# Optimization experiments

Measured on AMD Instinct MI355X. Metric: run time of the kernel, lower is better.

Reference implementation:

```python
import jax, jax.numpy as jnp
import numpy as np

D_MODEL = 512
N_HEADS = 8
MAX_CH = 128
LN_EPS = 1e-5


def setup_inputs() -> dict:
    key = jax.random.key(0)
    ks = jax.random.split(key, 8)
    B, T, C, D = 8, 256, 64, D_MODEL
    x = jax.random.normal(ks[0], (B, T, C, D), dtype=jnp.float32)
    # nn.MultiheadAttention params: packed in_proj [3D, D], out_proj [D, D]
    in_proj_w = jax.random.normal(ks[1], (3 * D, D), dtype=jnp.float32) * 0.02
    in_proj_b = jnp.zeros((3 * D,), dtype=jnp.float32)
    out_proj_w = jax.random.normal(ks[2], (D, D), dtype=jnp.float32) * 0.02
    out_proj_b = jnp.zeros((D,), dtype=jnp.float32)
    ln_g = jnp.ones((D,), dtype=jnp.float32)
    ln_b = jnp.zeros((D,), dtype=jnp.float32)
    rel_pos_bias = jax.random.normal(ks[3], (N_HEADS, MAX_CH, MAX_CH), dtype=jnp.float32) * 0.02
    return {"x": x, "in_proj_w": in_proj_w, "in_proj_b": in_proj_b,
            "out_proj_w": out_proj_w, "out_proj_b": out_proj_b,
            "ln_g": ln_g, "ln_b": ln_b, "rel_pos_bias": rel_pos_bias}


def _layernorm(x, g, b):
    mu = jnp.mean(x, axis=-1, keepdims=True)
    var = jnp.var(x, axis=-1, keepdims=True)
    return (x - mu) * jax.lax.rsqrt(var + LN_EPS) * g + b


def reference(x, in_proj_w, in_proj_b, out_proj_w, out_proj_b, ln_g, ln_b, rel_pos_bias):
    B, T, C, D = x.shape
    H = N_HEADS
    hd = D // H
    N = B * T
    xf = x.reshape(N, C, D)
    # 2D additive attn_mask: mean over heads of rel-pos bias, broadcast over heads/batch
    bias = jnp.mean(rel_pos_bias[:, :C, :C], axis=0)  # [C, C]
    qkv = xf @ in_proj_w.T + in_proj_b  # [N, C, 3D]
    q, k, v = jnp.split(qkv, 3, axis=-1)
    q = q.reshape(N, C, H, hd)
    k = k.reshape(N, C, H, hd)
    v = v.reshape(N, C, H, hd)
    scores = jnp.einsum('nqhd,nkhd->nhqk', q, k) / jnp.sqrt(jnp.float32(hd))
    scores = scores + bias[None, None, :, :]
    attn = jax.nn.softmax(scores, axis=-1)
    ctx = jnp.einsum('nhqk,nkhd->nqhd', attn, v).reshape(N, C, D)
    attn_out = ctx @ out_proj_w.T + out_proj_b
    out = _layernorm(xf + attn_out, ln_g, ln_b)
    return out.reshape(B, T, C, D)
```

## Files before the change

kernel.cpp:

```cpp
#include <hip/hip_runtime.h>
#include <stdint.h>
#include <stddef.h>


typedef __attribute__((ext_vector_type(8))) short short8;
typedef __attribute__((ext_vector_type(4))) float f32x4;

typedef __attribute__((address_space(3))) unsigned int as3_u32;
typedef __attribute__((address_space(1))) unsigned int as1_u32;

#define VMCNT12 asm volatile("s_waitcnt vmcnt(12)" ::: "memory")
#define VMCNT8 asm volatile("s_waitcnt vmcnt(8)" ::: "memory")
#define VMCNT5 asm volatile("s_waitcnt vmcnt(5)" ::: "memory")
#define VMCNT4 asm volatile("s_waitcnt vmcnt(4)" ::: "memory")
#define VMCNT0 asm volatile("s_waitcnt vmcnt(0)" ::: "memory")
#define LGKM0  asm volatile("s_waitcnt lgkmcnt(0)" ::: "memory")
#define BARR() __builtin_amdgcn_s_barrier()
#define PRIO1  __builtin_amdgcn_s_setprio(1)
#define PRIO0  __builtin_amdgcn_s_setprio(0)

__device__ __forceinline__ unsigned short f2bf(float f) {
  unsigned u = __builtin_bit_cast(unsigned, f);
  u = (u + 0x7FFFu + ((u >> 16) & 1u)) >> 16;
  return (unsigned short)u;
}

__device__ __forceinline__ f32x4 mfma16(short8 a, short8 b, f32x4 c) {
  return __builtin_amdgcn_mfma_f32_16x16x32_bf16(a, b, c, 0, 0, 0);
}

__device__ __forceinline__ short8 rd8s(const char* buf, int row, int unit) {
  return *(const short8*)(buf + row * 128 + ((unit ^ (row & 7)) * 16));
}
__device__ __forceinline__ void wr2s(char* buf, int row, int col, unsigned short v) {
  int slot = (col >> 3) ^ (row & 7);
  *(unsigned short*)(buf + row * 128 + slot * 16 + (col & 7) * 2) = v;
}
__device__ __forceinline__ void wr8s(char* buf, int row, int col, uint2 v) {
  int slot = (col >> 3) ^ (row & 7);
  *(uint2*)(buf + row * 128 + slot * 16 + (col & 7) * 2) = v;
}

__device__ __forceinline__ void stage16k(char* ldsbase, const char* gsrc, int w, int lane) {
#pragma unroll
  for (int j = 0; j < 4; ++j) {
    int off = j * 4096 + w * 1024;
    __builtin_amdgcn_global_load_lds((const as1_u32*)(gsrc + off + lane * 16),
                                     (as3_u32*)(ldsbase + off), 16, 0, 0);
  }
}

__device__ __forceinline__ void load_xq(short8* xq, const char* xqbase,
                                        int wm, int l15, int g) {
#pragma unroll
  for (int mt = 0; mt < 2; ++mt)
#pragma unroll
    for (int ks = 0; ks < 4; ++ks) {
      int row = wm * 32 + mt * 16 + l15;
      int u = ks * 4 + g;
      xq[mt * 4 + ks] = *(const short8*)(xqbase + u * 1024 + row * 16);
    }
}

__device__ __forceinline__ void proj_body(const char* ws, const short8* xq,
                                          int wn, int l15, int g, f32x4 acc[2][2]) {
  PRIO1;
#pragma unroll
  for (int ks = 0; ks < 4; ++ks)
#pragma unroll
    for (int nt = 0; nt < 2; ++nt) {
      int row = wn * 32 + nt * 16 + l15;
      int kg = ks * 4 + g;
      int us = (kg & 8) | ((kg ^ row) & 7);
      short8 bfr = *(const short8*)(ws + row * 256 + us * 16);
      acc[0][nt] = mfma16(xq[ks], bfr, acc[0][nt]);
      acc[1][nt] = mfma16(xq[4 + ks], bfr, acc[1][nt]);
    }
  PRIO0;
}

__global__ void prep_kernel(const float* __restrict__ x,
                            const float* __restrict__ wqkv_f,
                            const float* __restrict__ wo_f,
                            const float* __restrict__ rel,
                            unsigned short* __restrict__ wt,
                            float* __restrict__ bias2d,
                            char* __restrict__ dout) {
  int b = blockIdx.x, tid = threadIdx.x;
  if (b < 8192) {
    int n = b >> 2, kc = b & 3;
    unsigned short* dst =
        (unsigned short*)(dout + (size_t)n * 131072 + 65536 + kc * 16384);
    const float* src0 = x + (size_t)n * 32768 + kc * 128;
#pragma unroll
    for (int t = 0; t < 4; ++t) {
      int row = t * 16 + (tid >> 4);
      int u = tid & 15;
      const float* src = src0 + row * 512 + u * 8;
      float4 a = *(const float4*)src;
      float4 c = *(const float4*)(src + 4);
      unsigned p0 = (unsigned)f2bf(a.x) | ((unsigned)f2bf(a.y) << 16);
      unsigned p1 = (unsigned)f2bf(a.z) | ((unsigned)f2bf(a.w) << 16);
      unsigned p2 = (unsigned)f2bf(c.x) | ((unsigned)f2bf(c.y) << 16);
      unsigned p3 = (unsigned)f2bf(c.z) | ((unsigned)f2bf(c.w) << 16);
      *(uint4*)(dst + (u * 64 + row) * 8) = make_uint4(p0, p1, p2, p3);
    }
  } else if (b < 8320) {
    int cb = b - 8192;
    unsigned short* dst = wt + (size_t)cb * 8192;
#pragma unroll
    for (int t = 0; t < 4; ++t) {
      int u = t * 256 + tid;
      int row = u >> 4, us = u & 15;
      int kg = (us & 8) | ((us ^ row) & 7);
      const float* src;
      if (cb < 96) {
        int h = cb / 12, j = cb % 12;
        int kc = j / 3, rg = j % 3;
        src = wqkv_f + (size_t)(rg * 512 + h * 64 + row) * 512 + kc * 128 + kg * 8;
      } else {
        int cw = cb - 96;
        int kc = cw >> 3, ng = cw & 7;
        src = wo_f + (size_t)(ng * 64 + row) * 512 + kc * 128 + kg * 8;
      }
      float4 a = *(const float4*)src;
      float4 c = *(const float4*)(src + 4);
      unsigned p0 = (unsigned)f2bf(a.x) | ((unsigned)f2bf(a.y) << 16);
      unsigned p1 = (unsigned)f2bf(a.z) | ((unsigned)f2bf(a.w) << 16);
      unsigned p2 = (unsigned)f2bf(c.x) | ((unsigned)f2bf(c.y) << 16);
      unsigned p3 = (unsigned)f2bf(c.z) | ((unsigned)f2bf(c.w) << 16);
      *(uint4*)(dst + u * 8) = make_uint4(p0, p1, p2, p3);
    }
  } else {
    int idx = (b - 8320) * 256 + tid;
    int m = idx >> 6, nn = idx & 63;
    float s = 0.f;
#pragma unroll
    for (int hh = 0; hh < 8; ++hh) s += rel[hh * 16384 + m * 128 + nn];
    bias2d[idx] = s * 0.125f;
  }
}

__global__ __launch_bounds__(256, 2) void attn_qkv(
    const char* __restrict__ wq,
    const float* __restrict__ bqkv,
    const float* __restrict__ bias2d,
    char* __restrict__ ctxg) {
  extern __shared__ __attribute__((aligned(16))) char smem[];
  char* WR = smem;
  char* B0 = smem + 49152;
  char* B1 = smem + 57344;
  char* B2 = smem + 65536;
  float* BQ = (float*)(smem + 73728);

  const int n = blockIdx.x;
  const int tid = threadIdx.x;
  const int w = tid >> 6, lane = tid & 63;
  const int l15 = lane & 15, g = lane >> 4;
  const int wm = w >> 1, wn = w & 1;
  const int mrow = w * 16 + g * 4;
  const int wrow = w * 16 + l15;

  const char* xsrc = ctxg + (size_t)n * 131072 + 65536;

#pragma unroll
  for (int i = 0; i < 6; ++i) BQ[i * 256 + tid] = bqkv[i * 256 + tid];
  float b2d[16];
#pragma unroll
  for (int nt = 0; nt < 4; ++nt)
#pragma unroll
    for (int r = 0; r < 4; ++r)
      b2d[nt * 4 + r] = bias2d[(mrow + r) * 64 + nt * 16 + l15];
  VMCNT0; LGKM0; BARR();

  short8 xq[8];
  load_xq(xq, xsrc, wm, l15, g);
  stage16k(WR, wq, w, lane);

  for (int h = 0; h < 8; ++h) {
    f32x4 aq[2][2] = {}, ak[2][2] = {}, av[2][2] = {};
#pragma unroll
    for (int kc = 0; kc < 4; ++kc) {
      const int j = h * 12 + kc * 3;
      stage16k(WR + 16384, wq + (size_t)(j + 1) * 16384, w, lane);
      if (h == 0 && kc == 0) { VMCNT4; } else { VMCNT12; }
      BARR();
      proj_body(WR, xq, wn, l15, g, aq);
      stage16k(WR + 32768, wq + (size_t)(j + 2) * 16384, w, lane);
      VMCNT4; BARR();
      proj_body(WR + 16384, xq, wn, l15, g, ak);
      if (j + 3 < 96) {
        stage16k(WR, wq + (size_t)(j + 3) * 16384, w, lane);
        VMCNT4;
      } else {
        VMCNT0;
      }
      BARR();
      proj_body(WR + 32768, xq, wn, l15, g, av);
      if (!(h == 7 && kc == 3))
        load_xq(xq, xsrc + (size_t)((kc + 1) & 3) * 16384, wm, l15, g);
    }

    {
      float bq2[2], bk2[2], bv2[2];
#pragma unroll
      for (int nt = 0; nt < 2; ++nt) {
        int col = h * 64 + wn * 32 + nt * 16 + l15;
        bq2[nt] = BQ[col];
        bk2[nt] = BQ[512 + col];
        bv2[nt] = BQ[1024 + col];
      }
#pragma unroll
      for (int mt = 0; mt < 2; ++mt)
#pragma unroll
        for (int nt = 0; nt < 2; ++nt) {
          int rowb = wm * 32 + mt * 16 + g * 4;
          int col = wn * 32 + nt * 16 + l15;
#pragma unroll
          for (int r = 0; r < 4; ++r) {
            wr2s(B0, rowb + r, col, f2bf(aq[mt][nt][r] + bq2[nt]));
            wr2s(B1, rowb + r, col, f2bf(ak[mt][nt][r] + bk2[nt]));
          }
          unsigned short p0 = f2bf(av[mt][nt][0] + bv2[nt]);
          unsigned short p1 = f2bf(av[mt][nt][1] + bv2[nt]);
          unsigned short p2 = f2bf(av[mt][nt][2] + bv2[nt]);
          unsigned short p3 = f2bf(av[mt][nt][3] + bv2[nt]);
          unsigned lo = (unsigned)p0 | ((unsigned)p1 << 16);
          unsigned hi = (unsigned)p2 | ((unsigned)p3 << 16);
          wr8s(B2, col, rowb, make_uint2(lo, hi));
        }
    }
    LGKM0; BARR();

    {
      f32x4 sc[4] = {};
      short8 aq0 = rd8s(B0, wrow, g);
      short8 aq1 = rd8s(B0, wrow, 4 + g);
#pragma unroll
      for (int nt = 0; nt < 4; ++nt)
        sc[nt] = mfma16(aq0, rd8s(B1, nt * 16 + l15, g), sc[nt]);
#pragma unroll
      for (int nt = 0; nt < 4; ++nt)
        sc[nt] = mfma16(aq1, rd8s(B1, nt * 16 + l15, 4 + g), sc[nt]);
      float mx[4] = {-1e30f, -1e30f, -1e30f, -1e30f};
#pragma unroll
      for (int nt = 0; nt < 4; ++nt)
#pragma unroll
        for (int r = 0; r < 4; ++r) {
          float v = sc[nt][r] * 0.125f + b2d[nt * 4 + r];
          sc[nt][r] = v;
          mx[r] = fmaxf(mx[r], v);
        }
#pragma unroll
      for (int mk = 1; mk < 16; mk <<= 1)
#pragma unroll
        for (int r = 0; r < 4; ++r) mx[r] = fmaxf(mx[r], __shfl_xor(mx[r], mk));
      float sm[4] = {0.f, 0.f, 0.f, 0.f};
#pragma unroll
      for (int nt = 0; nt < 4; ++nt)
#pragma unroll
        for (int r = 0; r < 4; ++r) {
          float e = __expf(sc[nt][r] - mx[r]);
          sc[nt][r] = e;
          sm[r] += e;
        }
#pragma unroll
      for (int mk = 1; mk < 16; mk <<= 1)
#pragma unroll
        for (int r = 0; r < 4; ++r) sm[r] += __shfl_xor(sm[r], mk);
      float inv[4];
#pragma unroll
      for (int r = 0; r < 4; ++r) inv[r] = 1.0f / sm[r];
#pragma unroll
      for (int nt = 0; nt < 4; ++nt)
#pragma unroll
        for (int r = 0; r < 4; ++r)
          wr2s(B0, mrow + r, nt * 16 + l15, f2bf(sc[nt][r] * inv[r]));
    }

    f32x4 cv[4] = {};
    {
      short8 ap0 = rd8s(B0, wrow, g);
      short8 ap1 = rd8s(B0, wrow, 4 + g);
#pragma unroll
      for (int nt = 0; nt < 4; ++nt)
        cv[nt] = mfma16(ap0, rd8s(B2, nt * 16 + l15, g), cv[nt]);
#pragma unroll
      for (int nt = 0; nt < 4; ++nt)
        cv[nt] = mfma16(ap1, rd8s(B2, nt * 16 + l15, 4 + g), cv[nt]);
    }
    BARR();
#pragma unroll
    for (int nt = 0; nt < 4; ++nt)
#pragma unroll
      for (int r = 0; r < 4; ++r)
        wr2s(B1, mrow + r, nt * 16 + l15, f2bf(cv[nt][r]));
    LGKM0; BARR();

    {
      char* cdst = ctxg + (size_t)n * 131072 + h * 8192;
#pragma unroll
      for (int it = 0; it < 2; ++it) {
        int flat = it * 256 + tid;
        int row = flat >> 3, s = flat & 7;
        uint4 v = *(const uint4*)(B1 + row * 128 + s * 16);
        *(uint4*)(cdst + row * 128 + s * 16) = v;
      }
    }
  }
}

__global__ __launch_bounds__(256, 2) void oproj_ln(
    const char* __restrict__ ctxg,
    const char* __restrict__ wo,
    const float* __restrict__ bo,
    const float* __restrict__ x,
    const float* __restrict__ lng,
    const float* __restrict__ lnb,
    float* __restrict__ out) {
  __shared__ __attribute__((aligned(16))) char smem[65536];
  char* WB = smem;
  char* CB = smem + 32768;
  float* EP  = (float*)smem;
  float* SM1 = (float*)(smem + 32768);
  float* SM2 = (float*)(smem + 33408);

  const int n = blockIdx.x;
  const int tid = threadIdx.x;
  const int w = tid >> 6, lane = tid & 63;
  const int l15 = lane & 15, g = lane >> 4;
  const int um = w >> 1, un = w & 1;

  const char* cbase = ctxg + (size_t)n * 131072;

  stage16k(CB, cbase, w, lane);
  stage16k(WB, wo, w, lane);

  f32x4 acc[8][2][2] = {};

  for (int kc = 0; kc < 4; ++kc) {
    short8 actx[2][4];
#pragma unroll
    for (int ng = 0; ng < 8; ++ng) {
      int b = kc * 8 + ng;
      if (b < 31)
        stage16k(WB + (((b + 1) & 1) << 14), wo + (size_t)(b + 1) * 16384, w, lane);
      if ((ng & 1) == 0 && kc < 3) {
        int p = ng >> 1;
        int off = p * 4096 + w * 1024;
        __builtin_amdgcn_global_load_lds(
            (const as1_u32*)(cbase + (kc + 1) * 16384 + off + lane * 16),
            (as3_u32*)(CB + (((kc + 1) & 1) << 14) + off), 16, 0, 0);
      }
      if (b < 31) { VMCNT5; } else { VMCNT0; }
      BARR();
      const char* cb = CB + ((kc & 1) << 14);
      if (ng == 0) {
#pragma unroll
        for (int mt = 0; mt < 2; ++mt)
#pragma unroll
          for (int ks = 0; ks < 4; ++ks) {
            int row = um * 32 + mt * 16 + l15;
            int u = ks * 4 + g;
            actx[mt][ks] = *(const short8*)(cb + (u >> 3) * 8192 + row * 128 +
                                            (((u & 7) ^ (row & 7)) * 16));
          }
      }
      const char* ws = WB + ((b & 1) << 14);
      PRIO1;
#pragma unroll
      for (int ks = 0; ks < 4; ++ks) {
#pragma unroll
        for (int nt = 0; nt < 2; ++nt) {
          int row = un * 32 + nt * 16 + l15;
          int kg = ks * 4 + g;
          int us = (kg & 8) | ((kg ^ row) & 7);
          short8 bfr = *(const short8*)(ws + row * 256 + us * 16);
          acc[ng][0][nt] = mfma16(actx[0][ks], bfr, acc[ng][0][nt]);
          acc[ng][1][nt] = mfma16(actx[1][ks], bfr, acc[ng][1][nt]);
        }
      }
      PRIO0;
      BARR();
    }
  }

  VMCNT0;
  const float* xblk = x + (size_t)n * 32768;
  float* oblk = out + (size_t)n * 32768;
  float s1[2][4] = {}, s2[2][4] = {};

#pragma unroll
  for (int ng = 0; ng < 8; ++ng) {
#pragma unroll
    for (int t = 0; t < 4; ++t) {
      int flat = t * 256 + tid;
      int row = flat >> 4, f4 = flat & 15;
      float4 v = *(const float4*)(xblk + row * 512 + ng * 64 + f4 * 4);
      *(float4*)(EP + row * 68 + f4 * 4) = v;
    }
    LGKM0; BARR();
    float boA[2];
#pragma unroll
    for (int nt = 0; nt < 2; ++nt) boA[nt] = bo[ng * 64 + un * 32 + nt * 16 + l15];
#pragma unroll
    for (int mt = 0; mt < 2; ++mt)
#pragma unroll
      for (int nt = 0; nt < 2; ++nt)
#pragma unroll
        for (int r = 0; r < 4; ++r) {
          int row = um * 32 + mt * 16 + g * 4 + r;
          float xv = EP[row * 68 + un * 32 + nt * 16 + l15];
          float v = acc[ng][mt][nt][r] + boA[nt] + xv;
          acc[ng][mt][nt][r] = v;
          s1[mt][r] += v;
          s2[mt][r] += v * v;
        }
    LGKM0; BARR();
  }
#pragma unroll
  for (int mk = 1; mk < 16; mk <<= 1)
#pragma unroll
    for (int mt = 0; mt < 2; ++mt)
#pragma unroll
      for (int r = 0; r < 4; ++r) {
        s1[mt][r] += __shfl_xor(s1[mt][r], mk);
        s2[mt][r] += __shfl_xor(s2[mt][r], mk);
      }
  if (l15 == 0) {
#pragma unroll
    for (int mt = 0; mt < 2; ++mt)
#pragma unroll
      for (int r = 0; r < 4; ++r) {
        int row = um * 32 + mt * 16 + g * 4 + r;
        SM1[row * 2 + un] = s1[mt][r];
        SM2[row * 2 + un] = s2[mt][r];
      }
  }
  LGKM0; BARR();
  float mu[2][4], rs[2][4];
#pragma unroll
  for (int mt = 0; mt < 2; ++mt)
#pragma unroll
    for (int r = 0; r < 4; ++r) {
      int row = um * 32 + mt * 16 + g * 4 + r;
      float a1 = SM1[row * 2] + SM1[row * 2 + 1];
      float a2 = SM2[row * 2] + SM2[row * 2 + 1];
      float m = a1 * (1.0f / 512.0f);
      float var = a2 * (1.0f / 512.0f) - m * m;
      mu[mt][r] = m;
      rs[mt][r] = rsqrtf(var + 1e-5f);
    }
  BARR();
#pragma unroll
  for (int ng = 0; ng < 8; ++ng) {
    float lgA[2], lbA[2];
#pragma unroll
    for (int nt = 0; nt < 2; ++nt) {
      int col = ng * 64 + un * 32 + nt * 16 + l15;
      lgA[nt] = lng[col];
      lbA[nt] = lnb[col];
    }
#pragma unroll
    for (int mt = 0; mt < 2; ++mt)
#pragma unroll
      for (int nt = 0; nt < 2; ++nt)
#pragma unroll
        for (int r = 0; r < 4; ++r) {
          int row = um * 32 + mt * 16 + g * 4 + r;
          EP[row * 68 + un * 32 + nt * 16 + l15] =
              (acc[ng][mt][nt][r] - mu[mt][r]) * rs[mt][r] * lgA[nt] + lbA[nt];
        }
    LGKM0; BARR();
#pragma unroll
    for (int t = 0; t < 4; ++t) {
      int flat = t * 256 + tid;
      int row = flat >> 4, f4 = flat & 15;
      *(float4*)(oblk + row * 512 + ng * 64 + f4 * 4) =
          *(const float4*)(EP + row * 68 + f4 * 4);
    }
    BARR();
  }
}

extern "C" void kernel_launch(void* const* d_in, const int* in_sizes, int n_in,
                              void* d_out, int out_size, void* d_ws, size_t ws_size,
                              hipStream_t stream) {
  const float* x    = (const float*)d_in[0];
  const float* wqkv = (const float*)d_in[1];
  const float* bqkv = (const float*)d_in[2];
  const float* wo   = (const float*)d_in[3];
  const float* bo   = (const float*)d_in[4];
  const float* lng  = (const float*)d_in[5];
  const float* lnb  = (const float*)d_in[6];
  const float* rel  = (const float*)d_in[7];

  unsigned short* wt = (unsigned short*)d_ws;
  float* bias2d = (float*)((char*)d_ws + 128 * 16384);
  const char* wqc = (const char*)d_ws;
  const char* woc = (const char*)d_ws + 96 * 16384;

  hipFuncSetAttribute(reinterpret_cast<const void*>(attn_qkv),
                      hipFuncAttributeMaxDynamicSharedMemorySize, 79872);

  prep_kernel<<<8336, 256, 0, stream>>>(x, wqkv, wo, rel, wt, bias2d,
                                        (char*)d_out);
  attn_qkv<<<2048, 256, 79872, stream>>>(wqc, bqkv, bias2d, (char*)d_out);
  oproj_ln<<<2048, 256, 0, stream>>>((const char*)d_out, woc, bo, x, lng, lnb,
                                     (float*)d_out);
}
```

Measured before the change: 589.4 us.

## Shrink QKV weight ring to 8KB chunks and raise attention occupancy to three blocks

The QKV projection now streams 8KB K-chunks (64-wide K) through a 24KB LDS ring instead of 16KB chunks through 48KB. Each wave owns a full 64-row × 16-column tile and loads its activations directly from global memory per chunk. Bias values are read from global memory instead of an LDS copy, and the prep kernel emits the matching new weight and activation layouts. Total LDS drops to 48KB so launch bounds can request three blocks per CU. The trade-off is twice as many barriers and pipeline stages and more per-wave activation loads.

Result: slower. 1.186 ms (+101.2%).

```diff
diff --git a/kernel.cpp b/kernel.cpp
--- a/kernel.cpp
+++ b/kernel.cpp
@@ -9,15 +9,15 @@
 typedef __attribute__((address_space(3))) unsigned int as3_u32;
 typedef __attribute__((address_space(1))) unsigned int as1_u32;
 
-#define VMCNT12 asm volatile("s_waitcnt vmcnt(12)" ::: "memory")
-#define VMCNT8 asm volatile("s_waitcnt vmcnt(8)" ::: "memory")
-#define VMCNT5 asm volatile("s_waitcnt vmcnt(5)" ::: "memory")
-#define VMCNT4 asm volatile("s_waitcnt vmcnt(4)" ::: "memory")
-#define VMCNT0 asm volatile("s_waitcnt vmcnt(0)" ::: "memory")
-#define LGKM0  asm volatile("s_waitcnt lgkmcnt(0)" ::: "memory")
-#define BARR() __builtin_amdgcn_s_barrier()
-#define PRIO1  __builtin_amdgcn_s_setprio(1)
-#define PRIO0  __builtin_amdgcn_s_setprio(0)
+#define VMCNT10 asm volatile("s_waitcnt vmcnt(10)" ::: "memory")
+#define VMCNT5  asm volatile("s_waitcnt vmcnt(5)" ::: "memory")
+#define VMCNT2  asm volatile("s_waitcnt vmcnt(2)" ::: "memory")
+#define VMCNT0  asm volatile("s_waitcnt vmcnt(0)" ::: "memory")
+#define LGKM0   asm volatile("s_waitcnt lgkmcnt(0)" ::: "memory")
+#define BARR()  __builtin_amdgcn_s_barrier()
+#define SCHEDB  __builtin_amdgcn_sched_barrier(0)
+#define PRIO1   __builtin_amdgcn_s_setprio(1)
+#define PRIO0   __builtin_amdgcn_s_setprio(0)
 
 __device__ __forceinline__ unsigned short f2bf(float f) {
   unsigned u = __builtin_bit_cast(unsigned, f);
@@ -41,6 +41,15 @@
   *(uint2*)(buf + row * 128 + slot * 16 + (col & 7) * 2) = v;
 }
 
+__device__ __forceinline__ void stage8k(char* ldsbase, const char* gsrc, int w, int lane) {
+#pragma unroll
+  for (int j = 0; j < 2; ++j) {
+    int off = j * 4096 + w * 1024;
+    __builtin_amdgcn_global_load_lds((const as1_u32*)(gsrc + off + lane * 16),
+                                     (as3_u32*)(ldsbase + off), 16, 0, 0);
+  }
+}
+
 __device__ __forceinline__ void stage16k(char* ldsbase, const char* gsrc, int w, int lane) {
 #pragma unroll
   for (int j = 0; j < 4; ++j) {
@@ -48,35 +57,6 @@
     __builtin_amdgcn_global_load_lds((const as1_u32*)(gsrc + off + lane * 16),
                                      (as3_u32*)(ldsbase + off), 16, 0, 0);
   }
-}
-
-__device__ __forceinline__ void load_xq(short8* xq, const char* xqbase,
-                                        int wm, int l15, int g) {
-#pragma unroll
-  for (int mt = 0; mt < 2; ++mt)
-#pragma unroll
-    for (int ks = 0; ks < 4; ++ks) {
-      int row = wm * 32 + mt * 16 + l15;
-      int u = ks * 4 + g;
-      xq[mt * 4 + ks] = *(const short8*)(xqbase + u * 1024 + row * 16);
-    }
-}
-
-__device__ __forceinline__ void proj_body(const char* ws, const short8* xq,
-                                          int wn, int l15, int g, f32x4 acc[2][2]) {
-  PRIO1;
-#pragma unroll
-  for (int ks = 0; ks < 4; ++ks)
-#pragma unroll
-    for (int nt = 0; nt < 2; ++nt) {
-      int row = wn * 32 + nt * 16 + l15;
-      int kg = ks * 4 + g;
-      int us = (kg & 8) | ((kg ^ row) & 7);
-      short8 bfr = *(const short8*)(ws + row * 256 + us * 16);
-      acc[0][nt] = mfma16(xq[ks], bfr, acc[0][nt]);
-      acc[1][nt] = mfma16(xq[4 + ks], bfr, acc[1][nt]);
-    }
-  PRIO0;
 }
 
 __global__ void prep_kernel(const float* __restrict__ x,
@@ -88,47 +68,61 @@
                             char* __restrict__ dout) {
   int b = blockIdx.x, tid = threadIdx.x;
   if (b < 8192) {
-    int n = b >> 2, kc = b & 3;
-    unsigned short* dst =
-        (unsigned short*)(dout + (size_t)n * 131072 + 65536 + kc * 16384);
-    const float* src0 = x + (size_t)n * 32768 + kc * 128;
+    int n = b >> 2, p = b & 3;
+    char* dstb = dout + (size_t)n * 131072 + 65536;
+    const float* srcb = x + (size_t)n * 32768;
 #pragma unroll
     for (int t = 0; t < 4; ++t) {
-      int row = t * 16 + (tid >> 4);
-      int u = tid & 15;
-      const float* src = src0 + row * 512 + u * 8;
+      int flat = t * 256 + tid;
+      int c = p * 2 + (flat >> 9);
+      int r512 = flat & 511;
+      int row = r512 >> 3, u = r512 & 7;
+      const float* src = srcb + row * 512 + c * 64 + u * 8;
       float4 a = *(const float4*)src;
-      float4 c = *(const float4*)(src + 4);
+      float4 cc = *(const float4*)(src + 4);
       unsigned p0 = (unsigned)f2bf(a.x) | ((unsigned)f2bf(a.y) << 16);
       unsigned p1 = (unsigned)f2bf(a.z) | ((unsigned)f2bf(a.w) << 16);
-      unsigned p2 = (unsigned)f2bf(c.x) | ((unsigned)f2bf(c.y) << 16);
-      unsigned p3 = (unsigned)f2bf(c.z) | ((unsigned)f2bf(c.w) << 16);
-      *(uint4*)(dst + (u * 64 + row) * 8) = make_uint4(p0, p1, p2, p3);
+      unsigned p2 = (unsigned)f2bf(cc.x) | ((unsigned)f2bf(cc.y) << 16);
+      unsigned p3 = (unsigned)f2bf(cc.z) | ((unsigned)f2bf(cc.w) << 16);
+      *(uint4*)(dstb + c * 8192 + u * 1024 + row * 16) = make_uint4(p0, p1, p2, p3);
+    }
+  } else if (b < 8288) {
+    int cb2 = (b - 8192) * 2;
+#pragma unroll
+    for (int t = 0; t < 4; ++t) {
+      int flat = t * 256 + tid;
+      int c = cb2 + (flat >> 9);
+      int r512 = flat & 511;
+      int row = r512 >> 3, us = r512 & 7;
+      int kg = us ^ (row & 7);
+      int h = c / 24, j = c % 24;
+      int kc = j / 3, rg = j % 3;
+      const float* src =
+          wqkv_f + (size_t)(rg * 512 + h * 64 + row) * 512 + kc * 64 + kg * 8;
+      float4 a = *(const float4*)src;
+      float4 cc = *(const float4*)(src + 4);
+      unsigned p0 = (unsigned)f2bf(a.x) | ((unsigned)f2bf(a.y) << 16);
+      unsigned p1 = (unsigned)f2bf(a.z) | ((unsigned)f2bf(a.w) << 16);
+      unsigned p2 = (unsigned)f2bf(cc.x) | ((unsigned)f2bf(cc.y) << 16);
+      unsigned p3 = (unsigned)f2bf(cc.z) | ((unsigned)f2bf(cc.w) << 16);
+      *(uint4*)(wt + (size_t)c * 4096 + r512 * 8) = make_uint4(p0, p1, p2, p3);
     }
   } else if (b < 8320) {
-    int cb = b - 8192;
-    unsigned short* dst = wt + (size_t)cb * 8192;
+    int cw = b - 8288;
+    unsigned short* dst = wt + 786432 + (size_t)cw * 8192;
 #pragma unroll
     for (int t = 0; t < 4; ++t) {
       int u = t * 256 + tid;
       int row = u >> 4, us = u & 15;
       int kg = (us & 8) | ((us ^ row) & 7);
-      const float* src;
-      if (cb < 96) {
-        int h = cb / 12, j = cb % 12;
-        int kc = j / 3, rg = j % 3;
-        src = wqkv_f + (size_t)(rg * 512 + h * 64 + row) * 512 + kc * 128 + kg * 8;
-      } else {
-        int cw = cb - 96;
-        int kc = cw >> 3, ng = cw & 7;
-        src = wo_f + (size_t)(ng * 64 + row) * 512 + kc * 128 + kg * 8;
-      }
+      int kcw = cw >> 3, ng = cw & 7;
+      const float* src = wo_f + (size_t)(ng * 64 + row) * 512 + kcw * 128 + kg * 8;
       float4 a = *(const float4*)src;
-      float4 c = *(const float4*)(src + 4);
+      float4 cc = *(const float4*)(src + 4);
       unsigned p0 = (unsigned)f2bf(a.x) | ((unsigned)f2bf(a.y) << 16);
       unsigned p1 = (unsigned)f2bf(a.z) | ((unsigned)f2bf(a.w) << 16);
-      unsigned p2 = (unsigned)f2bf(c.x) | ((unsigned)f2bf(c.y) << 16);
-      unsigned p3 = (unsigned)f2bf(c.z) | ((unsigned)f2bf(c.w) << 16);
+      unsigned p2 = (unsigned)f2bf(cc.x) | ((unsigned)f2bf(cc.y) << 16);
+      unsigned p3 = (unsigned)f2bf(cc.z) | ((unsigned)f2bf(cc.w) << 16);
       *(uint4*)(dst + u * 8) = make_uint4(p0, p1, p2, p3);
     }
   } else {
@@ -141,94 +135,121 @@
   }
 }
 
-__global__ __launch_bounds__(256, 2) void attn_qkv(
+__global__ __launch_bounds__(256, 3) void attn_qkv(
     const char* __restrict__ wq,
     const float* __restrict__ bqkv,
     const float* __restrict__ bias2d,
     char* __restrict__ ctxg) {
-  extern __shared__ __attribute__((aligned(16))) char smem[];
-  char* WR = smem;
-  char* B0 = smem + 49152;
-  char* B1 = smem + 57344;
-  char* B2 = smem + 65536;
-  float* BQ = (float*)(smem + 73728);
+  __shared__ __attribute__((aligned(16))) char smem[49152];
+  char* RING = smem;
+  char* B0 = smem + 24576;
+  char* B1 = smem + 32768;
+  char* B2 = smem + 40960;
 
   const int n = blockIdx.x;
   const int tid = threadIdx.x;
   const int w = tid >> 6, lane = tid & 63;
   const int l15 = lane & 15, g = lane >> 4;
-  const int wm = w >> 1, wn = w & 1;
+  const int wn = w;
+  const int brow = wn * 16 + l15;
   const int mrow = w * 16 + g * 4;
   const int wrow = w * 16 + l15;
+  const int us0 = (g ^ (brow & 7)) * 16;
+  const int us1 = ((4 + g) ^ (brow & 7)) * 16;
 
   const char* xsrc = ctxg + (size_t)n * 131072 + 65536;
 
-#pragma unroll
-  for (int i = 0; i < 6; ++i) BQ[i * 256 + tid] = bqkv[i * 256 + tid];
   float b2d[16];
 #pragma unroll
   for (int nt = 0; nt < 4; ++nt)
 #pragma unroll
     for (int r = 0; r < 4; ++r)
       b2d[nt * 4 + r] = bias2d[(mrow + r) * 64 + nt * 16 + l15];
-  VMCNT0; LGKM0; BARR();
-
-  short8 xq[8];
-  load_xq(xq, xsrc, wm, l15, g);
-  stage16k(WR, wq, w, lane);
+  VMCNT0;
+
+  stage8k(RING, wq, w, lane);
 
   for (int h = 0; h < 8; ++h) {
-    f32x4 aq[2][2] = {}, ak[2][2] = {}, av[2][2] = {};
-#pragma unroll
-    for (int kc = 0; kc < 4; ++kc) {
-      const int j = h * 12 + kc * 3;
-      stage16k(WR + 16384, wq + (size_t)(j + 1) * 16384, w, lane);
-      if (h == 0 && kc == 0) { VMCNT4; } else { VMCNT12; }
-      BARR();
-      proj_body(WR, xq, wn, l15, g, aq);
-      stage16k(WR + 32768, wq + (size_t)(j + 2) * 16384, w, lane);
-      VMCNT4; BARR();
-      proj_body(WR + 16384, xq, wn, l15, g, ak);
-      if (j + 3 < 96) {
-        stage16k(WR, wq + (size_t)(j + 3) * 16384, w, lane);
-        VMCNT4;
+    f32x4 aq[4] = {}, ak[4] = {}, av[4] = {};
+#pragma unroll
+    for (int kc = 0; kc < 8; ++kc) {
+      const int cb = h * 24 + kc * 3;
+      short8 xa[8];
+#pragma unroll
+      for (int mt = 0; mt < 4; ++mt)
+#pragma unroll
+        for (int ks = 0; ks < 2; ++ks)
+          xa[mt * 2 + ks] = *(const short8*)(xsrc + kc * 8192 +
+                                             (ks * 4 + g) * 1024 +
+                                             (mt * 16 + l15) * 16);
+      SCHEDB;
+      stage8k(RING + 8192, wq + (size_t)(cb + 1) * 8192, w, lane);
+      VMCNT10; BARR();
+      {
+        short8 bf0 = *(const short8*)(RING + brow * 128 + us0);
+        short8 bf1 = *(const short8*)(RING + brow * 128 + us1);
+        PRIO1;
+#pragma unroll
+        for (int mt = 0; mt < 4; ++mt) {
+          aq[mt] = mfma16(xa[mt * 2], bf0, aq[mt]);
+          aq[mt] = mfma16(xa[mt * 2 + 1], bf1, aq[mt]);
+        }
+        PRIO0;
+      }
+      stage8k(RING + 16384, wq + (size_t)(cb + 2) * 8192, w, lane);
+      VMCNT2; BARR();
+      {
+        short8 bf0 = *(const short8*)(RING + 8192 + brow * 128 + us0);
+        short8 bf1 = *(const short8*)(RING + 8192 + brow * 128 + us1);
+        PRIO1;
+#pragma unroll
+        for (int mt = 0; mt < 4; ++mt) {
+          ak[mt] = mfma16(xa[mt * 2], bf0, ak[mt]);
+          ak[mt] = mfma16(xa[mt * 2 + 1], bf1, ak[mt]);
+        }
+        PRIO0;
+      }
+      if (cb + 3 < 192) {
+        stage8k(RING, wq + (size_t)(cb + 3) * 8192, w, lane);
+        VMCNT2;
       } else {
         VMCNT0;
       }
       BARR();
-      proj_body(WR + 32768, xq, wn, l15, g, av);
-      if (!(h == 7 && kc == 3))
-        load_xq(xq, xsrc + (size_t)((kc + 1) & 3) * 16384, wm, l15, g);
+      {
+        short8 bf0 = *(const short8*)(RING + 16384 + brow * 128 + us0);
+        short8 bf1 = *(const short8*)(RING + 16384 + brow * 128 + us1);
+        PRIO1;
+#pragma unroll
+        for (int mt = 0; mt < 4; ++mt) {
+          av[mt] = mfma16(xa[mt * 2], bf0, av[mt]);
+          av[mt] = mfma16(xa[mt * 2 + 1], bf1, av[mt]);
+        }
+        PRIO0;
+      }
     }
 
     {
-      float bq2[2], bk2[2], bv2[2];
-#pragma unroll
-      for (int nt = 0; nt < 2; ++nt) {
-        int col = h * 64 + wn * 32 + nt * 16 + l15;
-        bq2[nt] = BQ[col];
-        bk2[nt] = BQ[512 + col];
-        bv2[nt] = BQ[1024 + col];
-      }
-#pragma unroll
-      for (int mt = 0; mt < 2; ++mt)
-#pragma unroll
-        for (int nt = 0; nt < 2; ++nt) {
-          int rowb = wm * 32 + mt * 16 + g * 4;
-          int col = wn * 32 + nt * 16 + l15;
-#pragma unroll
-          for (int r = 0; r < 4; ++r) {
-            wr2s(B0, rowb + r, col, f2bf(aq[mt][nt][r] + bq2[nt]));
-            wr2s(B1, rowb + r, col, f2bf(ak[mt][nt][r] + bk2[nt]));
-          }
-          unsigned short p0 = f2bf(av[mt][nt][0] + bv2[nt]);
-          unsigned short p1 = f2bf(av[mt][nt][1] + bv2[nt]);
-          unsigned short p2 = f2bf(av[mt][nt][2] + bv2[nt]);
-          unsigned short p3 = f2bf(av[mt][nt][3] + bv2[nt]);
-          unsigned lo = (unsigned)p0 | ((unsigned)p1 << 16);
-          unsigned hi = (unsigned)p2 | ((unsigned)p3 << 16);
-          wr8s(B2, col, rowb, make_uint2(lo, hi));
-        }
+      int col = wn * 16 + l15;
+      float bq = bqkv[h * 64 + col];
+      float bk = bqkv[512 + h * 64 + col];
+      float bv = bqkv[1024 + h * 64 + col];
+#pragma unroll
+      for (int mt = 0; mt < 4; ++mt) {
+        int rowb = mt * 16 + g * 4;
+#pragma unroll
+        for (int r = 0; r < 4; ++r) {
+          wr2s(B0, rowb + r, col, f2bf(aq[mt][r] + bq));
+          wr2s(B1, rowb + r, col, f2bf(ak[mt][r] + bk));
+        }
+        unsigned short p0 = f2bf(av[mt][0] + bv);
+        unsigned short p1 = f2bf(av[mt][1] + bv);
+        unsigned short p2 = f2bf(av[mt][2] + bv);
+        unsigned short p3 = f2bf(av[mt][3] + bv);
+        unsigned lo = (unsigned)p0 | ((unsigned)p1 << 16);
+        unsigned hi = (unsigned)p2 | ((unsigned)p3 << 16);
+        wr8s(B2, col, rowb, make_uint2(lo, hi));
+      }
     }
     LGKM0; BARR();
 
@@ -496,16 +517,13 @@
   const float* rel  = (const float*)d_in[7];
 
   unsigned short* wt = (unsigned short*)d_ws;
-  float* bias2d = (float*)((char*)d_ws + 128 * 16384);
+  float* bias2d = (float*)((char*)d_ws + 2097152);
   const char* wqc = (const char*)d_ws;
-  const char* woc = (const char*)d_ws + 96 * 16384;
-
-  hipFuncSetAttribute(reinterpret_cast<const void*>(attn_qkv),
-                      hipFuncAttributeMaxDynamicSharedMemorySize, 79872);
+  const char* woc = (const char*)d_ws + 1572864;
 
   prep_kernel<<<8336, 256, 0, stream>>>(x, wqkv, wo, rel, wt, bias2d,
                                         (char*)d_out);
-  attn_qkv<<<2048, 256, 79872, stream>>>(wqc, bqkv, bias2d, (char*)d_out);
+  attn_qkv<<<2048, 256, 0, stream>>>(wqc, bqkv, bias2d, (char*)d_out);
   oproj_ln<<<2048, 256, 0, stream>>>((const char*)d_out, woc, bo, x, lng, lnb,
                                      (float*)d_out);
 }
```
